# Optimization experiments

Hardware: AMD Instinct MI355X
Metric: run time of the kernel (lower is better)

## Reference

```python
import jax, jax.numpy as jnp
import numpy as np


def log_g(x):
    # faithful to torch: where(x>=0, log(relu(x)+0.5), 5 - softplus(-x))
    return jnp.where(x >= 0, jnp.log(jax.nn.relu(x) + 0.5), 5.0 - jax.nn.softplus(-x))


def setup_inputs() -> dict:
    key = jax.random.key(0)
    ks = jax.random.split(key, 6)
    B, T, D, H = 8, 4096, 1024, 1024
    s = 1.0 / np.sqrt(D)
    return {
        "x": jax.random.normal(ks[0], (B, T, D), jnp.float32),
        "h_0": jax.random.normal(ks[1], (B, 1, H), jnp.float32),
        "Wz_w": jax.random.normal(ks[2], (D, H), jnp.float32) * s,
        "Wz_b": jax.random.normal(ks[3], (H,), jnp.float32) * 0.1,
        "Wh_w": jax.random.normal(ks[4], (D, H), jnp.float32) * s,
        "Wh_b": jax.random.normal(ks[5], (H,), jnp.float32) * 0.1,
    }


def reference(x, h_0, Wz_w, Wz_b, Wh_w, Wh_b):
    # k = W_z(x)
    k = jnp.einsum('btd,dh->bth', x, Wz_w) + Wz_b
    log_z = -jax.nn.softplus(-k)          # log sigmoid(k)
    log_coeffs = -jax.nn.softplus(k)      # log(1 - sigmoid(k))
    log_h0 = log_g(h_0)                                            # [B,1,H]
    log_tilde_h = log_g(jnp.einsum('btd,dh->bth', x, Wh_w) + Wh_b)  # [B,T,H]
    log_values = jnp.concatenate([log_h0, log_z + log_tilde_h], axis=1)  # [B,T+1,H]
    # a_star = pad(cumsum(log_coeffs, dim=1), (0,0,1,0)) -> one zero row at t=0
    a_star = jnp.pad(jnp.cumsum(log_coeffs, axis=1), ((0, 0), (1, 0), (0, 0)))  # [B,T+1,H]
    log_h = a_star + jax.lax.cumlogsumexp(log_values - a_star, axis=1)
    return jnp.exp(log_h)[:, 1:]  # [B,T,H]
```

## Files before the change

kernel.cpp:

```cpp
#include <hip/hip_runtime.h>
#include <hip/hip_bf16.h>
#include <stdint.h>

#define B_   8
#define T_   4096
#define D_   1024
#define H_   1024
#define M_   (B_ * T_)
#define NC_  64
#define TC_  64


typedef __attribute__((ext_vector_type(4))) float f32x4;
typedef __attribute__((ext_vector_type(8))) short bfr8;
typedef _Float16 f16;
typedef __attribute__((ext_vector_type(2))) _Float16 f16x2;

__device__ __forceinline__ unsigned short f2bf(float f) {
  unsigned int u = __float_as_uint(f);
  u += 0x7fffu + ((u >> 16) & 1u);
  return (unsigned short)(u >> 16);
}
__device__ __forceinline__ float bf2f(unsigned short h) {
  return __uint_as_float(((unsigned int)h) << 16);
}

__device__ __forceinline__ void gload16(const void* g, void* l) {
  __builtin_amdgcn_global_load_lds((const __attribute__((address_space(1))) void*)g,
                                   (__attribute__((address_space(3))) void*)l,
                                   16, 0, 0);
}

__device__ __forceinline__ float g_of(float hv) {
  return (hv >= 0.f) ? (hv + 0.5f)
                     : 148.4131591025766f / (1.f + __expf(-hv));
}

__global__ void prep_w(const float* __restrict__ Wz, const float* __restrict__ Wh,
                       unsigned short* __restrict__ wth, unsigned short* __restrict__ wtl,
                       float* __restrict__ whT, unsigned int* __restrict__ fcnt)
{
  if (blockIdx.x == 0 && blockIdx.y == 0 && threadIdx.x == 0) *fcnt = 0u;
  __shared__ float tile[32][33];
  int k0 = blockIdx.x * 32, n0 = blockIdx.y * 32;
  int tx = threadIdx.x & 31, ty = threadIdx.x >> 5;
  bool ish = (n0 >= 1024);
  const float* src = ish ? Wh : Wz;
  int nn0 = ish ? (n0 - 1024) : n0;
#pragma unroll
  for (int i = 0; i < 4; i++) {
    int k = k0 + ty * 4 + i;
    tile[ty * 4 + i][tx] = src[(size_t)k * 1024 + nn0 + tx];
  }
  __syncthreads();
#pragma unroll
  for (int i = 0; i < 4; i++) {
    int n = n0 + ty * 4 + i;
    float v = tile[tx][ty * 4 + i];
    unsigned short hi = f2bf(v);
    unsigned short lo = f2bf(v - bf2f(hi));
    wth[(size_t)n * 1024 + k0 + tx] = hi;
    wtl[(size_t)n * 1024 + k0 + tx] = lo;
    if (ish)
      whT[(size_t)(n - 1024) * 1024 + k0 + tx] = v;
  }
}

__global__ void split_x(const float* __restrict__ x,
                        unsigned short* __restrict__ xh,
                        unsigned short* __restrict__ xl)
{
  const size_t total = (size_t)M_ * D_;
  size_t i = ((size_t)blockIdx.x * 256 + threadIdx.x) * 8;
  const size_t stride = (size_t)gridDim.x * 256 * 8;
  for (; i < total; i += stride) {
    uint4 a = *(const uint4*)&x[i];
    uint4 b = *(const uint4*)&x[i + 4];
    unsigned int h01 = __builtin_amdgcn_perm(a.y, a.x, 0x07060302u);
    unsigned int h23 = __builtin_amdgcn_perm(a.w, a.z, 0x07060302u);
    unsigned int h45 = __builtin_amdgcn_perm(b.y, b.x, 0x07060302u);
    unsigned int h67 = __builtin_amdgcn_perm(b.w, b.z, 0x07060302u);
    float l0 = __uint_as_float(a.x) - __uint_as_float(a.x & 0xffff0000u);
    float l1 = __uint_as_float(a.y) - __uint_as_float(a.y & 0xffff0000u);
    float l2 = __uint_as_float(a.z) - __uint_as_float(a.z & 0xffff0000u);
    float l3 = __uint_as_float(a.w) - __uint_as_float(a.w & 0xffff0000u);
    float l4 = __uint_as_float(b.x) - __uint_as_float(b.x & 0xffff0000u);
    float l5 = __uint_as_float(b.y) - __uint_as_float(b.y & 0xffff0000u);
    float l6 = __uint_as_float(b.z) - __uint_as_float(b.z & 0xffff0000u);
    float l7 = __uint_as_float(b.w) - __uint_as_float(b.w & 0xffff0000u);
    unsigned int o01 = __builtin_amdgcn_perm(__float_as_uint(l1), __float_as_uint(l0), 0x07060302u);
    unsigned int o23 = __builtin_amdgcn_perm(__float_as_uint(l3), __float_as_uint(l2), 0x07060302u);
    unsigned int o45 = __builtin_amdgcn_perm(__float_as_uint(l5), __float_as_uint(l4), 0x07060302u);
    unsigned int o67 = __builtin_amdgcn_perm(__float_as_uint(l7), __float_as_uint(l6), 0x07060302u);
    *(uint4*)&xh[i] = make_uint4(h01, h23, h45, h67);
    *(uint4*)&xl[i] = make_uint4(o01, o23, o45, o67);
  }
}

__device__ __forceinline__ void epilogue_cv(
    const f32x4 (&accz)[4][2], const f32x4 (&acch)[4][2],
    int m0, int n0, int wr, int wc, int lrow, int lhalf, int lane,
    const float* __restrict__ bz, const float* __restrict__ bhb,
    f16x2* __restrict__ cvbuf,
    unsigned int* __restrict__ fcnt, unsigned int* __restrict__ flist,
    float* __restrict__ fsuf, unsigned int fcap,
    float* __restrict__ Cc, float* __restrict__ Vv)
{
#pragma unroll
  for (int j = 0; j < 2; j++) {
    int col = n0 + wc * 32 + j * 16 + lrow;
    float kb = bz[col], hb = bhb[col];
    float CC = 1.f, VV = 0.f;
    float SCs[4], gCs[4];
#pragma unroll
    for (int i = 0; i < 4; i++) {
      int row0 = m0 + wr * 64 + i * 16 + lhalf * 4;
      float SC = 1.f, SV = 0.f;
#pragma unroll
      for (int r = 0; r < 4; r++) {
        float kv = accz[i][j][r] + kb;
        float hv = acch[i][j][r] + hb;
        f16 kf = (f16)kv;
        float c  = 1.f / (1.f + __expf((float)kf));
        float v  = (1.f - c) * g_of(hv);
        size_t off = (size_t)(row0 + r) * H_ + col;
        f16x2 pr; pr[0] = kf; pr[1] = (f16)v;
        cvbuf[off] = pr;
        float vr = (float)pr[1];
        SV = fmaf(c, SV, vr);
        SC *= c;
      }
      float oC = __shfl_xor(SC, 16);
      float oV = __shfl_xor(SV, 16);
      float nC = SC * oC;
      float nV = (lane & 16) ? fmaf(SC, oV, SV)
                             : fmaf(oC, SV, oV);
      oC = __shfl_xor(nC, 32);
      oV = __shfl_xor(nV, 32);
      float gC = nC * oC;
      float gV = (lane & 32) ? fmaf(nC, oV, nV)
                             : fmaf(oC, nV, oV);
      VV = fmaf(gC, VV, gV);
      CC *= gC;
      SCs[i] = SC; gCs[i] = gC;
    }
    if (lane < 16) {
      int bb2 = m0 >> 12;
      int ch  = ((m0 & 4095) >> 6) + wr;
      size_t oo = ((size_t)bb2 * NC_ + ch) * H_ + col;
      Cc[oo] = CC; Vv[oo] = VV;
    }
    float gsuf3 = 1.f;
    float gsuf2 = gCs[3];
    float gsuf1 = gCs[2] * gCs[3];
    float gsuf0 = gCs[1] * gsuf1;
    float gsuf[4] = {gsuf0, gsuf1, gsuf2, gsuf3};
#pragma unroll
    for (int i = 0; i < 4; i++) {
      float a1 = __shfl(SCs[i], lrow + 16);
      float a2 = __shfl(SCs[i], lrow + 32);
      float a3 = __shfl(SCs[i], lrow + 48);
      float lh = 1.f;
      if (lhalf < 3) lh *= a3;
      if (lhalf < 2) lh *= a2;
      if (lhalf < 1) lh *= a1;
      float base = lh * gsuf[i];
      float cr[4], hv4[4];
#pragma unroll
      for (int r = 0; r < 4; r++) {
        float kv = accz[i][j][r] + kb;
        f16 kf = (f16)kv;
        cr[r]  = 1.f / (1.f + __expf((float)kf));
        hv4[r] = acch[i][j][r] + hb;
      }
      float rs1 = cr[2] * cr[3];
      float rs[4] = {cr[1] * rs1, rs1, cr[3], 1.f};
      int row0 = m0 + wr * 64 + i * 16 + lhalf * 4;
#pragma unroll
      for (int r = 0; r < 4; r++) {
        if (__builtin_fabsf(hv4[r]) < 1e-3f) {
          unsigned int p = atomicAdd(fcnt, 1u);
          if (p < fcap) {
            flist[p] = (unsigned int)((size_t)(row0 + r) * H_ + col);
            fsuf[p]  = rs[r] * base;
          }
        }
      }
    }
  }
}

__global__ __launch_bounds__(256, 2) void gemm_cv_s(
    const unsigned short* __restrict__ xh, const unsigned short* __restrict__ xl,
    const unsigned short* __restrict__ wth, const unsigned short* __restrict__ wtl,
    const float* __restrict__ bz, const float* __restrict__ bhb,
    f16x2* __restrict__ cvbuf,
    unsigned int* __restrict__ fcnt, unsigned int* __restrict__ flist,
    float* __restrict__ fsuf, unsigned int fcap,
    float* __restrict__ Cc, float* __restrict__ Vv)
{
  __shared__ __align__(16) unsigned short As_h[4096], As_l[4096];
  __shared__ __align__(16) unsigned short Bzh[2048], Bzl[2048];
  __shared__ __align__(16) unsigned short Bhh[2048], Bhl[2048];
  int tid = threadIdx.x;
  int lane = tid & 63, wv = tid >> 6;
  int wr = wv >> 1, wc = wv & 1;
  int lrow = lane & 15, lhalf = lane >> 4;

  int bid = blockIdx.x;
  int cpx = gridDim.x >> 3;
  int swz = (bid & 7) * cpx + (bid >> 3);
  int grp = swz >> 7, wi = swz & 127;
  int mt = grp * 8 + (wi & 7);
  int nt = wi >> 3;
  int m0 = mt * 128, n0 = nt * 64;

  f32x4 accz[4][2], acch[4][2];
#pragma unroll
  for (int i = 0; i < 4; i++)
#pragma unroll
    for (int j = 0; j < 2; j++) {
      accz[i][j] = (f32x4){0.f, 0.f, 0.f, 0.f};
      acch[i][j] = (f32x4){0.f, 0.f, 0.f, 0.f};
    }

  int alr = lane >> 2, akc = (lane & 3) * 8;
  const unsigned short* axh = xh + (size_t)(m0 + wv * 32 + alr) * D_ + akc;
  const unsigned short* axl = xl + (size_t)(m0 + wv * 32 + alr) * D_ + akc;
  int aldb = wv * 1024;
  int srow = tid >> 2, skb = (tid & 3) * 8;
  int blds = wv * 512;

  for (int k0 = 0; k0 < D_; k0 += 32) {
    gload16(axh + k0,            &As_h[aldb]);
    gload16(axh + 16 * D_ + k0,  &As_h[aldb + 512]);
    gload16(axl + k0,            &As_l[aldb]);
    gload16(axl + 16 * D_ + k0,  &As_l[aldb + 512]);
    {
      size_t gz = (size_t)(n0 + srow) * D_ + k0 + skb;
      size_t gh = (size_t)(1024 + n0 + srow) * D_ + k0 + skb;
      gload16(wth + gz, &Bzh[blds]);
      gload16(wtl + gz, &Bzl[blds]);
      gload16(wth + gh, &Bhh[blds]);
      gload16(wtl + gh, &Bhl[blds]);
    }
    __syncthreads();

    bfr8 ah[4], al[4], bzh[2], bzl[2], bhh[2], bhl[2];
    int ab = (wr * 64 + lrow) * 32 + lhalf * 8;
    int bb = (wc * 32 + lrow) * 32 + lhalf * 8;
#pragma unroll
    for (int f = 0; f < 4; f++) {
      ah[f] = *(const bfr8*)&As_h[ab + f * 512];
      al[f] = *(const bfr8*)&As_l[ab + f * 512];
    }
#pragma unroll
    for (int j = 0; j < 2; j++) {
      bzh[j] = *(const bfr8*)&Bzh[bb + j * 512];
      bzl[j] = *(const bfr8*)&Bzl[bb + j * 512];
      bhh[j] = *(const bfr8*)&Bhh[bb + j * 512];
      bhl[j] = *(const bfr8*)&Bhl[bb + j * 512];
    }
#pragma unroll
    for (int i = 0; i < 4; i++)
#pragma unroll
      for (int j = 0; j < 2; j++) {
        accz[i][j] = __builtin_amdgcn_mfma_f32_16x16x32_bf16(ah[i], bzh[j], accz[i][j], 0, 0, 0);
        accz[i][j] = __builtin_amdgcn_mfma_f32_16x16x32_bf16(al[i], bzh[j], accz[i][j], 0, 0, 0);
        accz[i][j] = __builtin_amdgcn_mfma_f32_16x16x32_bf16(ah[i], bzl[j], accz[i][j], 0, 0, 0);
        acch[i][j] = __builtin_amdgcn_mfma_f32_16x16x32_bf16(ah[i], bhh[j], acch[i][j], 0, 0, 0);
        acch[i][j] = __builtin_amdgcn_mfma_f32_16x16x32_bf16(al[i], bhh[j], acch[i][j], 0, 0, 0);
        acch[i][j] = __builtin_amdgcn_mfma_f32_16x16x32_bf16(ah[i], bhl[j], acch[i][j], 0, 0, 0);
      }
    __syncthreads();
  }

  epilogue_cv(accz, acch, m0, n0, wr, wc, lrow, lhalf, lane,
              bz, bhb, cvbuf, fcnt, flist, fsuf, fcap, Cc, Vv);
}

__global__ __launch_bounds__(256, 2) void gemm_cv(
    const float* __restrict__ x,
    const unsigned short* __restrict__ wth, const unsigned short* __restrict__ wtl,
    const float* __restrict__ bz, const float* __restrict__ bhb,
    f16x2* __restrict__ cvbuf,
    unsigned int* __restrict__ fcnt, unsigned int* __restrict__ flist,
    float* __restrict__ fsuf, unsigned int fcap,
    float* __restrict__ Cc, float* __restrict__ Vv)
{
  __shared__ __align__(16) unsigned short As_h[4096], As_l[4096];
  __shared__ __align__(16) unsigned short Bzh[2048], Bzl[2048];
  __shared__ __align__(16) unsigned short Bhh[2048], Bhl[2048];
  int tid = threadIdx.x;
  int lane = tid & 63, wv = tid >> 6;
  int wr = wv >> 1, wc = wv & 1;
  int lrow = lane & 15, lhalf = lane >> 4;

  int bid = blockIdx.x;
  int cpx = gridDim.x >> 3;
  int swz = (bid & 7) * cpx + (bid >> 3);
  int grp = swz >> 7, wi = swz & 127;
  int mt = grp * 8 + (wi & 7);
  int nt = wi >> 3;
  int m0 = mt * 128, n0 = nt * 64;

  f32x4 accz[4][2], acch[4][2];
#pragma unroll
  for (int i = 0; i < 4; i++)
#pragma unroll
    for (int j = 0; j < 2; j++) {
      accz[i][j] = (f32x4){0.f, 0.f, 0.f, 0.f};
      acch[i][j] = (f32x4){0.f, 0.f, 0.f, 0.f};
    }

  int art = tid >> 3, ac4 = (tid & 7) * 4;
  int srow = tid >> 2, skb = (tid & 3) * 8;
  int blds = wv * 512;

  for (int k0 = 0; k0 < D_; k0 += 32) {
#pragma unroll
    for (int p = 0; p < 4; p++) {
      int row = p * 32 + art;
      uint4 vu = *(const uint4*)&x[(size_t)(m0 + row) * D_ + k0 + ac4];
      unsigned int hi01 = __builtin_amdgcn_perm(vu.y, vu.x, 0x07060302u);
      unsigned int hi23 = __builtin_amdgcn_perm(vu.w, vu.z, 0x07060302u);
      float l0 = __uint_as_float(vu.x) - __uint_as_float(vu.x & 0xffff0000u);
      float l1 = __uint_as_float(vu.y) - __uint_as_float(vu.y & 0xffff0000u);
      float l2 = __uint_as_float(vu.z) - __uint_as_float(vu.z & 0xffff0000u);
      float l3 = __uint_as_float(vu.w) - __uint_as_float(vu.w & 0xffff0000u);
      unsigned int lo01 = __builtin_amdgcn_perm(__float_as_uint(l1),
                                                __float_as_uint(l0), 0x07060302u);
      unsigned int lo23 = __builtin_amdgcn_perm(__float_as_uint(l3),
                                                __float_as_uint(l2), 0x07060302u);
      *(uint2*)&As_h[row * 32 + ac4] = make_uint2(hi01, hi23);
      *(uint2*)&As_l[row * 32 + ac4] = make_uint2(lo01, lo23);
    }
    {
      size_t gz = (size_t)(n0 + srow) * D_ + k0 + skb;
      size_t gh = (size_t)(1024 + n0 + srow) * D_ + k0 + skb;
      gload16(wth + gz, &Bzh[blds]);
      gload16(wtl + gz, &Bzl[blds]);
      gload16(wth + gh, &Bhh[blds]);
      gload16(wtl + gh, &Bhl[blds]);
    }
    __syncthreads();

    bfr8 ah[4], al[4], bzh[2], bzl[2], bhh[2], bhl[2];
    int ab = (wr * 64 + lrow) * 32 + lhalf * 8;
    int bb = (wc * 32 + lrow) * 32 + lhalf * 8;
#pragma unroll
    for (int f = 0; f < 4; f++) {
      ah[f] = *(const bfr8*)&As_h[ab + f * 512];
      al[f] = *(const bfr8*)&As_l[ab + f * 512];
    }
#pragma unroll
    for (int j = 0; j < 2; j++) {
      bzh[j] = *(const bfr8*)&Bzh[bb + j * 512];
      bzl[j] = *(const bfr8*)&Bzl[bb + j * 512];
      bhh[j] = *(const bfr8*)&Bhh[bb + j * 512];
      bhl[j] = *(const bfr8*)&Bhl[bb + j * 512];
    }
#pragma unroll
    for (int i = 0; i < 4; i++)
#pragma unroll
      for (int j = 0; j < 2; j++) {
        accz[i][j] = __builtin_amdgcn_mfma_f32_16x16x32_bf16(ah[i], bzh[j], accz[i][j], 0, 0, 0);
        accz[i][j] = __builtin_amdgcn_mfma_f32_16x16x32_bf16(al[i], bzh[j], accz[i][j], 0, 0, 0);
        accz[i][j] = __builtin_amdgcn_mfma_f32_16x16x32_bf16(ah[i], bzl[j], accz[i][j], 0, 0, 0);
        acch[i][j] = __builtin_amdgcn_mfma_f32_16x16x32_bf16(ah[i], bhh[j], acch[i][j], 0, 0, 0);
        acch[i][j] = __builtin_amdgcn_mfma_f32_16x16x32_bf16(al[i], bhh[j], acch[i][j], 0, 0, 0);
        acch[i][j] = __builtin_amdgcn_mfma_f32_16x16x32_bf16(ah[i], bhl[j], acch[i][j], 0, 0, 0);
      }
    __syncthreads();
  }

  epilogue_cv(accz, acch, m0, n0, wr, wc, lrow, lhalf, lane,
              bz, bhb, cvbuf, fcnt, flist, fsuf, fcap, Cc, Vv);
}

__global__ void fixup_kc512(const float* __restrict__ x, const float* __restrict__ whT,
                            const float* __restrict__ bhb, f16x2* cvbuf,
                            const unsigned int* __restrict__ fcnt,
                            const unsigned int* __restrict__ flist,
                            const float* __restrict__ fsuf, unsigned int fcap,
                            float* __restrict__ Vv)
{
  unsigned int n = *fcnt; if (n > fcap) n = fcap;
  unsigned int gtid = blockIdx.x * blockDim.x + threadIdx.x;
  unsigned int nt = gridDim.x * blockDim.x;
  const unsigned int lim = (unsigned int)M_ * (unsigned int)H_;
  for (unsigned int i = gtid; i < n; i += nt) {
    unsigned int o = flist[i];
    if (o >= lim) continue;
    unsigned int row = o >> 10, col = o & 1023u;
    const float* xr = x + (size_t)row * D_;
    const float* wr = whT + (size_t)col * D_;
    float a1 = 0.f, a2 = 0.f;
    for (int d = 0; d < 512; d++)
      a1 = fmaf(xr[d], wr[d], a1);
    for (int d = 512; d < 1024; d++)
      a2 = fmaf(xr[d], wr[d], a2);
    float hs = (a1 + a2) + bhb[col];
    float g  = (hs >= 0.f) ? (hs + 0.5f)
                           : 148.4131591025766f / (1.f + __expf(-hs));
    f16x2 pr = cvbuf[o];
    float z  = 1.f / (1.f + __expf(-(float)pr[0]));
    float vold = (float)pr[1];
    pr[1] = (f16)(z * g);
    cvbuf[o] = pr;
    float dv = (float)pr[1] - vold;
    if (dv != 0.f) {
      unsigned int b = row >> 12, ch = (row >> 6) & 63u;
      atomicAdd(&Vv[((size_t)b * NC_ + ch) * H_ + col], fsuf[i] * dv);
    }
  }
}

__global__ void scan_p2(const float* __restrict__ h0, const float* __restrict__ Cc,
                        const float* __restrict__ Vv, float* __restrict__ Hi)
{
  int idx = blockIdx.x * 256 + threadIdx.x;
  float hs = g_of(h0[idx]);
  int b = idx >> 10, h = idx & 1023;
  for (int ch = 0; ch < NC_; ch++) {
    size_t o = ((size_t)b * NC_ + ch) * H_ + h;
    Hi[o] = hs;
    hs = fmaf(Cc[o], hs, Vv[o]);
  }
}

__global__ void scan_p3(void* buf, const float* __restrict__ Hi)
{
  __shared__ f16x2 S[TC_][256];
  const f16x2* cv = (const f16x2*)buf;
  float* out = (float*)buf;
  int t = threadIdx.x;
  int hg = blockIdx.x, ch = blockIdx.y, b = blockIdx.z;
  int col = hg * 256 + t;
  size_t base = ((size_t)b * T_ + (size_t)ch * TC_) * H_ + col;
#pragma unroll 4
  for (int r = 0; r < TC_; r++)
    S[r][t] = cv[base + (size_t)r * H_];
  __syncthreads();
  float hs = Hi[((size_t)b * NC_ + ch) * H_ + col];
#pragma unroll 4
  for (int r = 0; r < TC_; r++) {
    f16x2 p = S[r][t];
    float c = 1.f / (1.f + __expf((float)p[0]));
    hs = fmaf(c, hs, (float)p[1]);
    out[base + (size_t)r * H_] = hs;
  }
}

extern "C" void kernel_launch(void* const* d_in, const int* in_sizes, int n_in,
                              void* d_out, int out_size, void* d_ws, size_t ws_size,
                              hipStream_t stream)
{
  const float* x  = (const float*)d_in[0];
  const float* h0 = (const float*)d_in[1];
  const float* Wz = (const float*)d_in[2];
  const float* bz = (const float*)d_in[3];
  const float* Wh = (const float*)d_in[4];
  const float* bh = (const float*)d_in[5];
  char* ws = (char*)d_ws;

  const size_t MiB = 1024u * 1024u;
  unsigned int* fcnt  = (unsigned int*)(ws);
  unsigned int* flist = (unsigned int*)(ws + 4096);
  float*        fsuf  = (float*)(ws + 1 * MiB);
  const unsigned int fcap = 192u * 1024u;
  unsigned short* wth = (unsigned short*)(ws + 2 * MiB);
  unsigned short* wtl = (unsigned short*)(ws + 6 * MiB);
  float* Cc = (float*)(ws + 10 * MiB);
  float* Vv = (float*)(ws + 12 * MiB);
  float* Hi = (float*)(ws + 14 * MiB);
  float* whT = (float*)(ws + 16 * MiB);
  unsigned short* xh = (unsigned short*)(ws + 20 * MiB);
  unsigned short* xl = (unsigned short*)(ws + 84 * MiB);
  const bool use_split = (ws_size >= 148 * MiB);

  f16x2* cvbuf = (f16x2*)d_out;

  prep_w<<<dim3(32, 64), 256, 0, stream>>>(Wz, Wh, wth, wtl, whT, fcnt);
  if (use_split) {
    split_x<<<2048, 256, 0, stream>>>(x, xh, xl);
    gemm_cv_s<<<4096, 256, 0, stream>>>(xh, xl, wth, wtl, bz, bh, cvbuf,
                                        fcnt, flist, fsuf, fcap, Cc, Vv);
  } else {
    gemm_cv<<<4096, 256, 0, stream>>>(x, wth, wtl, bz, bh, cvbuf,
                                      fcnt, flist, fsuf, fcap, Cc, Vv);
  }
  fixup_kc512<<<512, 256, 0, stream>>>(x, whT, bh, cvbuf,
                                       fcnt, flist, fsuf, fcap, Vv);
  scan_p2<<<32, 256, 0, stream>>>(h0, Cc, Vv, Hi);
  scan_p3<<<dim3(4, 64, 8), 256, 0, stream>>>(d_out, Hi);
}
```

Before: 699.6 us.

## Widen split-GEMM tile to 128x128 per block to improve operand reuse

The split-precision GEMM now computes a 128x128 output tile per block instead of 128x64, so each wave owns 4x4 fragments and the grid halves to 2048 blocks. Each A-tile load from LDS now feeds twice as many MFMAs, and global traffic for x per output column falls. The tile-to-block mapping is reworked to match, and the epilogue is templated on the fragment count. The cost is doubled accumulator registers (128 floats of accumulators per thread) and doubled B shared memory, which may spill or lower occupancy under launch_bounds(256,2). The split_x launch count is also doubled.

```diff
diff --git a/kernel.cpp b/kernel.cpp
--- a/kernel.cpp
+++ b/kernel.cpp
@@ -97,8 +97,9 @@
   }
 }
 
+template <int NJ>
 __device__ __forceinline__ void epilogue_cv(
-    const f32x4 (&accz)[4][2], const f32x4 (&acch)[4][2],
+    const f32x4 (&accz)[4][NJ], const f32x4 (&acch)[4][NJ],
     int m0, int n0, int wr, int wc, int lrow, int lhalf, int lane,
     const float* __restrict__ bz, const float* __restrict__ bhb,
     f16x2* __restrict__ cvbuf,
@@ -107,8 +108,8 @@
     float* __restrict__ Cc, float* __restrict__ Vv)
 {
 #pragma unroll
-  for (int j = 0; j < 2; j++) {
-    int col = n0 + wc * 32 + j * 16 + lrow;
+  for (int j = 0; j < NJ; j++) {
+    int col = n0 + wc * (NJ * 16) + j * 16 + lrow;
     float kb = bz[col], hb = bhb[col];
     float CC = 1.f, VV = 0.f;
     float SCs[4], gCs[4];
@@ -190,7 +191,7 @@
   }
 }
 
-__global__ __launch_bounds__(256, 2) void gemm_cv_s(
+__global__ __launch_bounds__(256, 2) void gemm_cv_w(
     const unsigned short* __restrict__ xh, const unsigned short* __restrict__ xl,
     const unsigned short* __restrict__ wth, const unsigned short* __restrict__ wtl,
     const float* __restrict__ bz, const float* __restrict__ bhb,
@@ -200,8 +201,8 @@
     float* __restrict__ Cc, float* __restrict__ Vv)
 {
   __shared__ __align__(16) unsigned short As_h[4096], As_l[4096];
-  __shared__ __align__(16) unsigned short Bzh[2048], Bzl[2048];
-  __shared__ __align__(16) unsigned short Bhh[2048], Bhl[2048];
+  __shared__ __align__(16) unsigned short Bzh[4096], Bzl[4096];
+  __shared__ __align__(16) unsigned short Bhh[4096], Bhl[4096];
   int tid = threadIdx.x;
   int lane = tid & 63, wv = tid >> 6;
   int wr = wv >> 1, wc = wv & 1;
@@ -210,16 +211,16 @@
   int bid = blockIdx.x;
   int cpx = gridDim.x >> 3;
   int swz = (bid & 7) * cpx + (bid >> 3);
-  int grp = swz >> 7, wi = swz & 127;
-  int mt = grp * 8 + (wi & 7);
-  int nt = wi >> 3;
-  int m0 = mt * 128, n0 = nt * 64;
-
-  f32x4 accz[4][2], acch[4][2];
+  int grp = swz >> 6, wi = swz & 63;
+  int mt = grp * 8 + (wi >> 3);
+  int nt = wi & 7;
+  int m0 = mt * 128, n0 = nt * 128;
+
+  f32x4 accz[4][4], acch[4][4];
 #pragma unroll
   for (int i = 0; i < 4; i++)
 #pragma unroll
-    for (int j = 0; j < 2; j++) {
+    for (int j = 0; j < 4; j++) {
       accz[i][j] = (f32x4){0.f, 0.f, 0.f, 0.f};
       acch[i][j] = (f32x4){0.f, 0.f, 0.f, 0.f};
     }
@@ -231,52 +232,58 @@
   int srow = tid >> 2, skb = (tid & 3) * 8;
   int blds = wv * 512;
 
+  int ab = (wr * 64 + lrow) * 32 + lhalf * 8;
+  int bb = (wc * 64 + lrow) * 32 + lhalf * 8;
+
   for (int k0 = 0; k0 < D_; k0 += 32) {
-    gload16(axh + k0,            &As_h[aldb]);
-    gload16(axh + 16 * D_ + k0,  &As_h[aldb + 512]);
-    gload16(axl + k0,            &As_l[aldb]);
-    gload16(axl + 16 * D_ + k0,  &As_l[aldb + 512]);
+    gload16(axh + k0,           &As_h[aldb]);
+    gload16(axh + 16 * D_ + k0, &As_h[aldb + 512]);
+    gload16(axl + k0,           &As_l[aldb]);
+    gload16(axl + 16 * D_ + k0, &As_l[aldb + 512]);
     {
-      size_t gz = (size_t)(n0 + srow) * D_ + k0 + skb;
-      size_t gh = (size_t)(1024 + n0 + srow) * D_ + k0 + skb;
-      gload16(wth + gz, &Bzh[blds]);
-      gload16(wtl + gz, &Bzl[blds]);
-      gload16(wth + gh, &Bhh[blds]);
-      gload16(wtl + gh, &Bhl[blds]);
+      size_t g1 = (size_t)(n0 + srow) * D_ + k0 + skb;
+      size_t g2 = (size_t)(n0 + 64 + srow) * D_ + k0 + skb;
+      size_t h1 = g1 + (size_t)1024 * D_;
+      size_t h2 = g2 + (size_t)1024 * D_;
+      gload16(wth + g1, &Bzh[blds]);
+      gload16(wth + g2, &Bzh[2048 + blds]);
+      gload16(wtl + g1, &Bzl[blds]);
+      gload16(wtl + g2, &Bzl[2048 + blds]);
+      gload16(wth + h1, &Bhh[blds]);
+      gload16(wth + h2, &Bhh[2048 + blds]);
+      gload16(wtl + h1, &Bhl[blds]);
+      gload16(wtl + h2, &Bhl[2048 + blds]);
     }
     __syncthreads();
 
-    bfr8 ah[4], al[4], bzh[2], bzl[2], bhh[2], bhl[2];
-    int ab = (wr * 64 + lrow) * 32 + lhalf * 8;
-    int bb = (wc * 32 + lrow) * 32 + lhalf * 8;
+    bfr8 ah[4], al[4];
 #pragma unroll
     for (int f = 0; f < 4; f++) {
       ah[f] = *(const bfr8*)&As_h[ab + f * 512];
       al[f] = *(const bfr8*)&As_l[ab + f * 512];
     }
 #pragma unroll
-    for (int j = 0; j < 2; j++) {
-      bzh[j] = *(const bfr8*)&Bzh[bb + j * 512];
-      bzl[j] = *(const bfr8*)&Bzl[bb + j * 512];
-      bhh[j] = *(const bfr8*)&Bhh[bb + j * 512];
-      bhl[j] = *(const bfr8*)&Bhl[bb + j * 512];
-    }
-#pragma unroll
-    for (int i = 0; i < 4; i++)
-#pragma unroll
-      for (int j = 0; j < 2; j++) {
-        accz[i][j] = __builtin_amdgcn_mfma_f32_16x16x32_bf16(ah[i], bzh[j], accz[i][j], 0, 0, 0);
-        accz[i][j] = __builtin_amdgcn_mfma_f32_16x16x32_bf16(al[i], bzh[j], accz[i][j], 0, 0, 0);
-        accz[i][j] = __builtin_amdgcn_mfma_f32_16x16x32_bf16(ah[i], bzl[j], accz[i][j], 0, 0, 0);
-        acch[i][j] = __builtin_amdgcn_mfma_f32_16x16x32_bf16(ah[i], bhh[j], acch[i][j], 0, 0, 0);
-        acch[i][j] = __builtin_amdgcn_mfma_f32_16x16x32_bf16(al[i], bhh[j], acch[i][j], 0, 0, 0);
-        acch[i][j] = __builtin_amdgcn_mfma_f32_16x16x32_bf16(ah[i], bhl[j], acch[i][j], 0, 0, 0);
+    for (int j = 0; j < 4; j++) {
+      int o = bb + j * 512;
+      bfr8 bzhj = *(const bfr8*)&Bzh[o];
+      bfr8 bzlj = *(const bfr8*)&Bzl[o];
+      bfr8 bhhj = *(const bfr8*)&Bhh[o];
+      bfr8 bhlj = *(const bfr8*)&Bhl[o];
+#pragma unroll
+      for (int i = 0; i < 4; i++) {
+        accz[i][j] = __builtin_amdgcn_mfma_f32_16x16x32_bf16(ah[i], bzhj, accz[i][j], 0, 0, 0);
+        accz[i][j] = __builtin_amdgcn_mfma_f32_16x16x32_bf16(al[i], bzhj, accz[i][j], 0, 0, 0);
+        accz[i][j] = __builtin_amdgcn_mfma_f32_16x16x32_bf16(ah[i], bzlj, accz[i][j], 0, 0, 0);
+        acch[i][j] = __builtin_amdgcn_mfma_f32_16x16x32_bf16(ah[i], bhhj, acch[i][j], 0, 0, 0);
+        acch[i][j] = __builtin_amdgcn_mfma_f32_16x16x32_bf16(al[i], bhhj, acch[i][j], 0, 0, 0);
+        acch[i][j] = __builtin_amdgcn_mfma_f32_16x16x32_bf16(ah[i], bhlj, acch[i][j], 0, 0, 0);
       }
+    }
     __syncthreads();
   }
 
-  epilogue_cv(accz, acch, m0, n0, wr, wc, lrow, lhalf, lane,
-              bz, bhb, cvbuf, fcnt, flist, fsuf, fcap, Cc, Vv);
+  epilogue_cv<4>(accz, acch, m0, n0, wr, wc, lrow, lhalf, lane,
+                 bz, bhb, cvbuf, fcnt, flist, fsuf, fcap, Cc, Vv);
 }
 
 __global__ __launch_bounds__(256, 2) void gemm_cv(
@@ -374,8 +381,8 @@
     __syncthreads();
   }
 
-  epilogue_cv(accz, acch, m0, n0, wr, wc, lrow, lhalf, lane,
-              bz, bhb, cvbuf, fcnt, flist, fsuf, fcap, Cc, Vv);
+  epilogue_cv<2>(accz, acch, m0, n0, wr, wc, lrow, lhalf, lane,
+                 bz, bhb, cvbuf, fcnt, flist, fsuf, fcap, Cc, Vv);
 }
 
 __global__ void fixup_kc512(const float* __restrict__ x, const float* __restrict__ whT,
@@ -483,8 +490,8 @@
 
   prep_w<<<dim3(32, 64), 256, 0, stream>>>(Wz, Wh, wth, wtl, whT, fcnt);
   if (use_split) {
-    split_x<<<2048, 256, 0, stream>>>(x, xh, xl);
-    gemm_cv_s<<<4096, 256, 0, stream>>>(xh, xl, wth, wtl, bz, bh, cvbuf,
+    split_x<<<4096, 256, 0, stream>>>(x, xh, xl);
+    gemm_cv_w<<<2048, 256, 0, stream>>>(xh, xl, wth, wtl, bz, bh, cvbuf,
                                         fcnt, flist, fsuf, fcap, Cc, Vv);
   } else {
     gemm_cv<<<4096, 256, 0, stream>>>(x, wth, wtl, bz, bh, cvbuf,
```

After: 766.5 us. 1.1x slower.
